# Performance work log

Measured on AMD Instinct MI355X. Metric: run time of the kernel, lower is better.

Reference implementation:

```python
import jax, jax.numpy as jnp
import numpy as np

IMG_H = IMG_W = 800
SIZES = (32, 64, 128, 256, 512)
FEAT_SHAPES = ((200, 200), (100, 100), (50, 50), (25, 25), (13, 13))
ASPECTS = np.array([0.5, 1.0, 2.0], np.float32)
MIN_SIZE = 10.0 / 1000.0
PRE_NMS = 4000
POST_NMS = 1000
IOU_TH = 0.7


def conv2d(x, w, b, pad):
    y = jax.lax.conv_general_dilated(
        x, w, window_strides=(1, 1), padding=[(pad, pad), (pad, pad)],
        dimension_numbers=("NCHW", "OIHW", "NCHW"))
    return y + b[None, :, None, None]


def make_anchors():
    # replicates torchvision AnchorGenerator: per-level single size, 3 aspect ratios
    out = []
    for (gh, gw), s in zip(FEAT_SHAPES, SIZES):
        h_r = np.sqrt(ASPECTS)
        w_r = 1.0 / h_r
        ws = s * w_r
        hs = s * h_r
        base = np.round(np.stack([-ws, -hs, ws, hs], 1) / 2.0)  # [3,4]
        stride_h = IMG_H // gh
        stride_w = IMG_W // gw
        sy = np.arange(gh, dtype=np.float32) * stride_h
        sx = np.arange(gw, dtype=np.float32) * stride_w
        yy, xx = np.meshgrid(sy, sx, indexing="ij")
        shifts = np.stack([xx, yy, xx, yy], axis=-1).reshape(-1, 1, 4)
        out.append((shifts + base[None]).reshape(-1, 4))
    a = np.concatenate(out, 0).astype(np.float32)
    a /= np.array([IMG_W, IMG_H, IMG_W, IMG_H], np.float32)  # normalize to [0,1]
    return jnp.asarray(a)


def xy_to_cxcy(a):
    return jnp.concatenate([(a[:, 2:] + a[:, :2]) / 2, a[:, 2:] - a[:, :2]], 1)


def cxcy_to_xy(a):
    return jnp.concatenate([a[:, :2] - a[:, 2:] / 2, a[:, :2] + a[:, 2:] / 2], 1)


def decode(t, anc):
    return jnp.concatenate([t[:, :2] * anc[:, 2:] + anc[:, :2],
                            jnp.exp(t[:, 2:]) * anc[:, 2:]], 1)


def rpn_head(feat, w_i, b_i, w_c, b_c, w_r, b_r):
    B = feat.shape[0]
    h = jax.nn.relu(conv2d(feat, w_i, b_i, 1))
    c = conv2d(h, w_c, b_c, 0).transpose(0, 2, 3, 1).reshape(B, -1, 2)
    r = conv2d(h, w_r, b_r, 0).transpose(0, 2, 3, 1).reshape(B, -1, 4)
    return c, r


def pairwise_iou(b):
    # b: [N,4] xyxy
    area = jnp.clip(b[:, 2] - b[:, 0], 0) * jnp.clip(b[:, 3] - b[:, 1], 0)
    lt = jnp.maximum(b[:, None, :2], b[None, :, :2])
    rb = jnp.minimum(b[:, None, 2:], b[None, :, 2:])
    wh = jnp.clip(rb - lt, 0)
    inter = wh[..., 0] * wh[..., 1]
    union = area[:, None] + area[None, :] - inter
    return jnp.where(union > 0, inter / union, 0.0)


def greedy_nms(ious, init_keep):
    N = ious.shape[0]
    idxs = jnp.arange(N)

    def body(i, keep):
        sup = keep[i] & (ious[i] > IOU_TH) & (idxs > i)
        return keep & ~sup

    return jax.lax.fori_loop(0, N, body, init_keep)


def rpn_forward(x, feats, w_inter, b_inter, w_cls, b_cls, w_reg, b_reg):
    cls_l, reg_l = [], []
    for f in feats:
        c, r = rpn_head(f, w_inter, b_inter, w_cls, b_cls, w_reg, b_reg)
        cls_l.append(c)
        reg_l.append(r)
    pred_cls = jnp.concatenate(cls_l, 1).reshape(-1, 2)   # [A,2]
    pred_reg = jnp.concatenate(reg_l, 1).reshape(-1, 4)   # [A,4]

    anchor = make_anchors()                               # [A,4] xyxy in [0,1]
    scores = jax.nn.softmax(pred_cls, axis=-1)[:, 1]
    roi = cxcy_to_xy(decode(pred_reg, xy_to_cxcy(anchor))).clip(0.0, 1.0)

    ws = roi[:, 2] - roi[:, 0]
    hs = roi[:, 3] - roi[:, 1]
    valid = (hs >= MIN_SIZE) & (ws >= MIN_SIZE)
    scores = jnp.where(valid, scores, -jnp.inf)

    top_scores, top_idx = jax.lax.top_k(scores, PRE_NMS)
    boxes = roi[top_idx]
    finite = jnp.isfinite(top_scores)
    boxes = jnp.where(finite[:, None], boxes, 0.0)  # neutralize filtered boxes

    ious = pairwise_iou(boxes)
    keep = greedy_nms(ious, finite)
    order = jnp.argsort(jnp.where(keep, jnp.arange(PRE_NMS), PRE_NMS + jnp.arange(PRE_NMS)))
    n_keep = jnp.minimum(keep.sum(), POST_NMS)
    sel = boxes[order[:POST_NMS]]
    roi_out = jnp.where(jnp.arange(POST_NMS)[:, None] < n_keep, sel, 0.0)  # padded [1000,4]
    return pred_cls, pred_reg, roi_out, anchor


def setup_inputs() -> dict:
    key = jax.random.key(0)
    ks = jax.random.split(key, 10)
    inp = {"x": jax.random.normal(ks[0], (1, 3, IMG_H, IMG_W), jnp.float32)}
    for i, (gh, gw) in enumerate(FEAT_SHAPES):
        inp[f"feat{i}"] = jax.random.normal(ks[1 + i], (1, 256, gh, gw), jnp.float32)
    # normal_init(m, 0, 0.01)
    inp["w_inter"] = jax.random.normal(ks[6], (256, 256, 3, 3), jnp.float32) * 0.01
    inp["b_inter"] = jnp.zeros((256,), jnp.float32)
    inp["w_cls"] = jax.random.normal(ks[7], (6, 256, 1, 1), jnp.float32) * 0.01
    inp["b_cls"] = jnp.zeros((6,), jnp.float32)
    inp["w_reg"] = jax.random.normal(ks[8], (12, 256, 1, 1), jnp.float32) * 0.01
    inp["b_reg"] = jnp.zeros((12,), jnp.float32)
    return inp


def reference(x, feat0, feat1, feat2, feat3, feat4,
              w_inter, b_inter, w_cls, b_cls, w_reg, b_reg):
    feats = [feat0, feat1, feat2, feat3, feat4]
    return rpn_forward(x, feats, w_inter, b_inter, w_cls, b_cls, w_reg, b_reg)
```

## Files before the change

kernel.cpp:

```cpp
#include <hip/hip_runtime.h>
#include <cmath>
#include <cstdint>

typedef unsigned int u32;
typedef unsigned long long u64;
typedef float v2f __attribute__((ext_vector_type(2)));

#define A_TOT   159882
#define PRE_NMS 4000
#define POST_NMS 1000
#define NWORDS  63
#define HIST_BINS 131072
#define HIST2_BINS 32768
#define SURV_CAP 8192
#define MONO_NEG_INF 0x007FFFFFu

struct BaseTab { float v[60]; };

__device__ inline u32 mono32f(float s) {
    u32 u = __float_as_uint(s);
    return (u & 0x80000000u) ? ~u : (u | 0x80000000u);
}

__device__ inline float pexp_f(float x0) {
    float x = fminf(x0, 88.3762626647950f);
    x = fmaxf(x, -88.3762626647949f);
    float m = floorf(__builtin_fmaf(x, 1.44269504088896341f, 0.5f));
    float r = __builtin_fmaf(m, -0.693359375f, x);
    r = __builtin_fmaf(m, 2.12194440e-4f, r);
    float z = r * r;
    float y = 1.9875691500E-4f;
    y = __builtin_fmaf(y, r, 1.3981999507E-3f);
    y = __builtin_fmaf(y, r, 8.3334519073E-3f);
    y = __builtin_fmaf(y, r, 4.1665795894E-2f);
    y = __builtin_fmaf(y, r, 1.6666665459E-1f);
    y = __builtin_fmaf(y, r, 5.0000001201E-1f);
    y = __builtin_fmaf(y, z, r);
    y = y + 1.0f;
    return ldexpf(y, (int)m);
}

__device__ inline float4 decode_box(const float* __restrict__ reg,
                                    const float* __restrict__ anc,
                                    u32 i, bool* valid) {
#pragma clang fp contract(off)
    float x1 = anc[4 * i], y1 = anc[4 * i + 1], x2 = anc[4 * i + 2], y2 = anc[4 * i + 3];
    float acx = (x2 + x1) / 2.0f, acy = (y2 + y1) / 2.0f;
    float aw = x2 - x1, ah = y2 - y1;
    float t0 = reg[4 * i], t1 = reg[4 * i + 1], t2 = reg[4 * i + 2], t3 = reg[4 * i + 3];
    float cx = (t0 * aw) + acx;
    float cy = (t1 * ah) + acy;
    float w  = pexp_f(t2) * aw;
    float hh = pexp_f(t3) * ah;
    float bx1 = fminf(fmaxf(cx - w / 2.0f, 0.f), 1.f);
    float by1 = fminf(fmaxf(cy - hh / 2.0f, 0.f), 1.f);
    float bx2 = fminf(fmaxf(cx + w / 2.0f, 0.f), 1.f);
    float by2 = fminf(fmaxf(cy + hh / 2.0f, 0.f), 1.f);
    float wsz = bx2 - bx1, hsz = by2 - by1;
    *valid = (hsz >= 0.01f) && (wsz >= 0.01f);
    return make_float4(bx1, by1, bx2, by2);
}

__device__ inline v2f pk_mul_blo(v2f a, v2f b) {
    v2f d;
    asm("v_pk_mul_f32 %0, %1, %2 op_sel:[0,0] op_sel_hi:[1,0]"
        : "=v"(d) : "v"(a), "v"(b));
    return d;
}
__device__ inline v2f pk_mul_bhi(v2f a, v2f b) {
    v2f d;
    asm("v_pk_mul_f32 %0, %1, %2 op_sel:[0,1] op_sel_hi:[1,1]"
        : "=v"(d) : "v"(a), "v"(b));
    return d;
}
__device__ inline v2f pk_add(v2f a, v2f b) {
    v2f d;
    asm("v_pk_add_f32 %0, %1, %2" : "=v"(d) : "v"(a), "v"(b));
    return d;
}

__device__ inline void gload16(const float* g, void* lds) {
    __builtin_amdgcn_global_load_lds(
        (const __attribute__((address_space(1))) void*)g,
        (__attribute__((address_space(3))) void*)lds,
        16, 0, 0);
}

__global__ __launch_bounds__(256) void wt_k(const float* __restrict__ w,
                                            float* __restrict__ Wt) {
    int i = blockIdx.x * 256 + threadIdx.x;
    if (i >= 2304 * 256) return;
    int co = i & 255, knew = i >> 8;
    int g = knew >> 8;
    int c = knew & 255;
    Wt[knew * 256 + co] = w[co * 2304 + c * 9 + g];
}

struct ConvMap {
    const float* feat[5];
    float* part[5];
    const float* Wt;
    const float* bias;
    u64 M[5];
    int bstart[6];
    int st[5], gh[5], gw[5], S[5], npan[5], fuse[5];
};

__global__ __launch_bounds__(256, 4) void conv_all(ConvMap cm)
{
#pragma clang fp contract(off)
    __shared__ float Ws[2][32][128];
    __shared__ float Xs[2][32][32];
    const int t  = threadIdx.x;
    const int cg = t & 31, xg = t >> 5;
    const int bid = blockIdx.x;
    const int l = (bid >= cm.bstart[1]) + (bid >= cm.bstart[2]) +
                  (bid >= cm.bstart[3]) + (bid >= cm.bstart[4]);
    const int local = bid - cm.bstart[l];
    const int st = cm.st[l], gh = cm.gh[l], gw = cm.gw[l];
    const int S = cm.S[l], npan = cm.npan[l];
    const float* __restrict__ feat = cm.feat[l];
    const float* __restrict__ Wt   = cm.Wt;
    float* __restrict__ part = cm.part[l];
    const int tile = local % st;
    const int zc   = local / st;
    const int s0   = tile * 32;
    const int z2 = zc & 1, pslot = zc >> 1;
    const int pb   = pslot * npan;
    const int send = (pb + npan) * 9;

    const u32 y00 = (u32)(((u64)(u32)s0 * cm.M[l]) >> 48);
    const int x00 = s0 - (int)y00 * gw;
    int xq = x00 + cg;
    int yq = (int)y00;
#pragma unroll
    for (int r = 0; r < 3; ++r) { if (xq >= gw) { xq -= gw; ++yq; } }

    const int srow0 = t >> 5;
    const int wcol  = (t & 31) << 2;
    const int wvoff = (t >> 6) * 1024;

    float px0, px1, px2, px3;

#define ISSUE_X(s_) do {                                                       \
        int g_  = (s_) >> 3, cb_ = ((s_) & 7) << 5;                            \
        int ky_ = g_ / 3, kx_ = g_ - ky_ * 3;                                  \
        int yy_ = yq + ky_ - 1;                                                \
        int xx_ = xq + kx_ - 1;                                                \
        bool ok_ = (yy_ >= 0) && (yy_ < gh) && (xx_ >= 0) && (xx_ < gw);       \
        int yyc_ = ok_ ? yy_ : 0;                                              \
        int xcc_ = ok_ ? xx_ : 0;                                              \
        const float* xsrc_ = feat + ((size_t)(cb_ + srow0) * gh + yyc_) * gw   \
                                  + xcc_;                                      \
        size_t xstr_ = (size_t)(8 * gh) * gw;                                  \
        float xa_ = xsrc_[0];                                                  \
        float xb_ = xsrc_[xstr_];                                              \
        float xc2_ = xsrc_[2 * xstr_];                                         \
        float xd_ = xsrc_[3 * xstr_];                                          \
        px0 = ok_ ? xa_ : 0.f;                                                 \
        px1 = ok_ ? xb_ : 0.f;                                                 \
        px2 = ok_ ? xc2_ : 0.f;                                                \
        px3 = ok_ ? xd_ : 0.f;                                                 \
    } while (0)

#define COMMIT_X(b_) do {                                                      \
        Xs[b_][srow0][cg]      = px0;                                          \
        Xs[b_][srow0 + 8][cg]  = px1;                                          \
        Xs[b_][srow0 + 16][cg] = px2;                                          \
        Xs[b_][srow0 + 24][cg] = px3;                                          \
    } while (0)

#define ISSUE_W(s_, b_) do {                                                   \
        int g_  = (s_) >> 3, cb_ = ((s_) & 7) << 5;                            \
        const float* wsrc_ = Wt + ((size_t)(g_ * 256 + cb_ + srow0) * 256)     \
                               + z2 * 128 + wcol;                              \
        char* ldsW_ = (char*)(&Ws[b_][0][0]) + wvoff;                          \
        gload16(wsrc_,        ldsW_);                                          \
        gload16(wsrc_ + 2048, ldsW_ + 4096);                                   \
        gload16(wsrc_ + 4096, ldsW_ + 8192);                                   \
        gload16(wsrc_ + 6144, ldsW_ + 12288);                                  \
    } while (0)

    v2f tA0=(v2f)0.f, tA1=(v2f)0.f, tA2=(v2f)0.f, tA3=(v2f)0.f;
    v2f tB0=(v2f)0.f, tB1=(v2f)0.f, tB2=(v2f)0.f, tB3=(v2f)0.f;

    const int sfirst = pb * 9;
    ISSUE_X(sfirst);
    COMMIT_X(0);
    ISSUE_W(sfirst, 0);
    ISSUE_X(sfirst + 1);
    __syncthreads();
    int cur = 0;

    for (int pi = pb; pi < pb + npan; ++pi) {
        v2f pA0=(v2f)0.f, pA1=(v2f)0.f, pA2=(v2f)0.f, pA3=(v2f)0.f;
        v2f pB0=(v2f)0.f, pB1=(v2f)0.f, pB2=(v2f)0.f, pB3=(v2f)0.f;
        for (int j = 0; j < 9; ++j) {
            int s = pi * 9 + j;
            int nxt = cur ^ 1;
            bool more = (s + 1 < send);
            if (more) {
                COMMIT_X(nxt);
                ISSUE_W(s + 1, nxt);
                if (s + 2 < send) ISSUE_X(s + 2);
            }
            const float* Wb = &Ws[cur][0][0];
            const float* Xb = &Xs[cur][0][0];
#pragma unroll 4
            for (int kk = 0; kk < 32; ++kk) {
                float4 xv = *(const float4*)(Xb + kk * 32 + xg * 4);
                v2f xlo; xlo[0] = xv.x; xlo[1] = xv.y;
                v2f xhi; xhi[0] = xv.z; xhi[1] = xv.w;
                v2f wA = *(const v2f*)(Wb + kk * 128 + cg * 2);
                pA0 = pk_add(pA0, pk_mul_blo(wA, xlo));
                pA1 = pk_add(pA1, pk_mul_bhi(wA, xlo));
                pA2 = pk_add(pA2, pk_mul_blo(wA, xhi));
                pA3 = pk_add(pA3, pk_mul_bhi(wA, xhi));
                v2f wB = *(const v2f*)(Wb + kk * 128 + 64 + cg * 2);
                pB0 = pk_add(pB0, pk_mul_blo(wB, xlo));
                pB1 = pk_add(pB1, pk_mul_bhi(wB, xlo));
                pB2 = pk_add(pB2, pk_mul_blo(wB, xhi));
                pB3 = pk_add(pB3, pk_mul_bhi(wB, xhi));
            }
            if (more) {
                __syncthreads();
                cur = nxt;
            }
        }
        tA0 = pk_add(tA0, pA0); tA1 = pk_add(tA1, pA1);
        tA2 = pk_add(tA2, pA2); tA3 = pk_add(tA3, pA3);
        tB0 = pk_add(tB0, pB0); tB1 = pk_add(tB1, pB1);
        tB2 = pk_add(tB2, pB2); tB3 = pk_add(tB3, pB3);
    }
#undef ISSUE_X
#undef COMMIT_X
#undef ISSUE_W
    const int c0 = z2 * 128 + cg * 2;
    if (cm.fuse[l]) {
        const float* bias = cm.bias;
        float bA0 = bias[c0], bA1 = bias[c0 + 1];
        float bB0 = bias[c0 + 64], bB1 = bias[c0 + 65];
        tA0[0] = fmaxf(tA0[0] + bA0, 0.f); tA0[1] = fmaxf(tA0[1] + bA1, 0.f);
        tA1[0] = fmaxf(tA1[0] + bA0, 0.f); tA1[1] = fmaxf(tA1[1] + bA1, 0.f);
        tA2[0] = fmaxf(tA2[0] + bA0, 0.f); tA2[1] = fmaxf(tA2[1] + bA1, 0.f);
        tA3[0] = fmaxf(tA3[0] + bA0, 0.f); tA3[1] = fmaxf(tA3[1] + bA1, 0.f);
        tB0[0] = fmaxf(tB0[0] + bB0, 0.f); tB0[1] = fmaxf(tB0[1] + bB1, 0.f);
        tB1[0] = fmaxf(tB1[0] + bB0, 0.f); tB1[1] = fmaxf(tB1[1] + bB1, 0.f);
        tB2[0] = fmaxf(tB2[0] + bB0, 0.f); tB2[1] = fmaxf(tB2[1] + bB1, 0.f);
        tB3[0] = fmaxf(tB3[0] + bB0, 0.f); tB3[1] = fmaxf(tB3[1] + bB1, 0.f);
    }
    float* op = part + (size_t)pslot * 256 * S;
    {
        int sp = s0 + xg * 4;
        size_t rA0 = (size_t)c0 * S + sp;
        size_t rA1 = rA0 + S;
        if (sp + 0 < S) { op[rA0 + 0] = tA0[0]; op[rA1 + 0] = tA0[1]; }
        if (sp + 1 < S) { op[rA0 + 1] = tA1[0]; op[rA1 + 1] = tA1[1]; }
        if (sp + 2 < S) { op[rA0 + 2] = tA2[0]; op[rA1 + 2] = tA2[1]; }
        if (sp + 3 < S) { op[rA0 + 3] = tA3[0]; op[rA1 + 3] = tA3[1]; }
        size_t rB0 = rA0 + (size_t)64 * S;
        size_t rB1 = rB0 + S;
        if (sp + 0 < S) { op[rB0 + 0] = tB0[0]; op[rB1 + 0] = tB0[1]; }
        if (sp + 1 < S) { op[rB0 + 1] = tB1[0]; op[rB1 + 1] = tB1[1]; }
        if (sp + 2 < S) { op[rB0 + 2] = tB2[0]; op[rB1 + 2] = tB2[1]; }
        if (sp + 3 < S) { op[rB0 + 3] = tB3[0]; op[rB1 + 3] = tB3[1]; }
    }
}

struct HeadMap {
    const float* h[5];
    int S[5], abase[5], npan[5], bstart[6];
};

__global__ __launch_bounds__(256) void head_all(
    HeadMap hm, const float* __restrict__ wc,
    const float* __restrict__ bc, const float* __restrict__ wr,
    const float* __restrict__ br, const float* __restrict__ bias,
    float* __restrict__ cls_out, float* __restrict__ reg_out)
{
#pragma clang fp contract(off)
    int bid = blockIdx.x;
    int l = (bid >= hm.bstart[1]) + (bid >= hm.bstart[2]) +
            (bid >= hm.bstart[3]) + (bid >= hm.bstart[4]);
    int local = bid - hm.bstart[l];
    const float* __restrict__ h = hm.h[l];
    const int S = hm.S[l];
    const int abase = hm.abase[l];
    const int npan = hm.npan[l];
    int s = local * 256 + threadIdx.x;
    if (s >= S) return;
    float ac[6]  = {0.f};
    float ar[12] = {0.f};
    for (int c = 0; c < 256; ++c) {
        size_t i = (size_t)c * S + s;
        float v;
        if (npan == 1) {
            v = h[i];
        } else {
            float vv = h[i];
            for (int p = 1; p < 8; ++p)
                vv = vv + h[(size_t)p * 256 * S + i];
            v = fmaxf(vv + bias[c], 0.f);
        }
#pragma unroll
        for (int ch = 0; ch < 6; ++ch) {
            float prod = wc[ch * 256 + c] * v;
            ac[ch] = ac[ch] + prod;
        }
#pragma unroll
        for (int ch = 0; ch < 12; ++ch) {
            float prod = wr[ch * 256 + c] * v;
            ar[ch] = ar[ch] + prod;
        }
    }
    long b2 = (long)abase + (long)s * 3;
#pragma unroll
    for (int a = 0; a < 3; ++a) {
#pragma unroll
        for (int c2 = 0; c2 < 2; ++c2)
            cls_out[(b2 + a) * 2 + c2] = ac[a * 2 + c2] + bc[a * 2 + c2];
#pragma unroll
        for (int d = 0; d < 4; ++d)
            reg_out[(b2 + a) * 4 + d] = ar[a * 4 + d] + br[a * 4 + d];
    }
}

__global__ __launch_bounds__(256) void score_k(
    const float* __restrict__ cls, const float* __restrict__ reg,
    BaseTab bt, u64* __restrict__ keys, u32* __restrict__ hist,
    float* __restrict__ anc_out)
{
#pragma clang fp contract(off)
    int i = blockIdx.x * 256 + threadIdx.x;
    if (i >= A_TOT) return;
    int l, base, gw, str;
    if (i < 120000)      { l = 0; base = 0;      gw = 200; str = 4;  }
    else if (i < 150000) { l = 1; base = 120000; gw = 100; str = 8;  }
    else if (i < 157500) { l = 2; base = 150000; gw = 50;  str = 16; }
    else if (i < 159375) { l = 3; base = 157500; gw = 25;  str = 32; }
    else                 { l = 4; base = 159375; gw = 13;  str = 61; }
    int j = i - base;
    int sj = j / 3;
    int a = j - sj * 3;
    int yy = sj / gw;
    int xx = sj - yy * gw;
    float sx = (float)(xx * str), sy = (float)(yy * str);
    const float* bb = &bt.v[(l * 3 + a) * 4];
    float a0 = (sx + bb[0]) / 800.0f;
    float a1 = (sy + bb[1]) / 800.0f;
    float a2 = (sx + bb[2]) / 800.0f;
    float a3 = (sy + bb[3]) / 800.0f;
    anc_out[4 * i + 0] = a0;
    anc_out[4 * i + 1] = a1;
    anc_out[4 * i + 2] = a2;
    anc_out[4 * i + 3] = a3;
    float l0 = cls[2 * i], l1 = cls[2 * i + 1];
    float m  = fmaxf(l0, l1);
    float e0 = pexp_f(l0 - m);
    float e1 = pexp_f(l1 - m);
    float sum = e0 + e1;
    float sc  = e1 / sum;
    float acx = (a2 + a0) / 2.0f, acy = (a3 + a1) / 2.0f;
    float aw = a2 - a0, ah = a3 - a1;
    float t0 = reg[4 * i], t1 = reg[4 * i + 1], t2 = reg[4 * i + 2], t3 = reg[4 * i + 3];
    float cx = (t0 * aw) + acx;
    float cy = (t1 * ah) + acy;
    float w  = pexp_f(t2) * aw;
    float hh = pexp_f(t3) * ah;
    float bx1 = fminf(fmaxf(cx - w / 2.0f, 0.f), 1.f);
    float by1 = fminf(fmaxf(cy - hh / 2.0f, 0.f), 1.f);
    float bx2 = fminf(fmaxf(cx + w / 2.0f, 0.f), 1.f);
    float by2 = fminf(fmaxf(cy + hh / 2.0f, 0.f), 1.f);
    float wsz = bx2 - bx1, hsz = by2 - by1;
    bool valid = (hsz >= 0.01f) && (wsz >= 0.01f);

    float score = valid ? sc : -INFINITY;
    u32 u = mono32f(score);
    keys[i] = ((u64)u << 32) | (u32)(~(u32)i);
    atomicAdd(&hist[u >> 15], 1u);
}

__global__ __launch_bounds__(1024) void topk_thresh(const u32* __restrict__ hist,
                                                    u32* __restrict__ counters) {
    __shared__ u32 part[1024];
    int t = threadIdx.x;
    u32 s = 0;
    for (int q = 0; q < 128; ++q) s += hist[HIST_BINS - 1 - (t * 128 + q)];
    part[t] = s;
    __syncthreads();
    if (t == 0) {
        u32 cum = 0, cumBefore = 0;
        int tc = 1023;
        for (int c = 0; c < 1024; ++c) {
            if (cum + part[c] >= PRE_NMS) { tc = c; cumBefore = cum; break; }
            cum += part[c];
        }
        u32 cum2 = cumBefore;
        int bstar = 0;
        for (int q = 0; q < 128; ++q) {
            int b = HIST_BINS - 1 - (tc * 128 + q);
            u32 hv = hist[b];
            if (cum2 + hv >= PRE_NMS) { bstar = b; break; }
            cum2 += hv;
        }
        counters[0] = (u32)bstar;
        counters[1] = cum2;
    }
}

__global__ __launch_bounds__(256) void hist2_k(const u64* __restrict__ keys,
                                               const u32* __restrict__ counters,
                                               u32* __restrict__ hist2) {
    int i = blockIdx.x * 256 + threadIdx.x;
    if (i >= A_TOT) return;
    u32 u = (u32)(keys[i] >> 32);
    if ((u >> 15) == counters[0]) atomicAdd(&hist2[u & 0x7FFF], 1u);
}

__global__ __launch_bounds__(1024) void thresh2_k(const u32* __restrict__ hist2,
                                                  u32* __restrict__ counters) {
    __shared__ u32 part[1024];
    int t = threadIdx.x;
    u32 s = 0;
    for (int q = 0; q < 32; ++q) s += hist2[HIST2_BINS - 1 - (t * 32 + q)];
    part[t] = s;
    __syncthreads();
    if (t == 0) {
        u32 bstar = counters[0];
        u32 cum = counters[1];
        int tc = 1023;
        u32 cumBefore = cum;
        for (int c = 0; c < 1024; ++c) {
            if (cum + part[c] >= PRE_NMS) { tc = c; cumBefore = cum; break; }
            cum += part[c];
        }
        u32 cum2 = cumBefore;
        u32 low = 0;
        for (int q = 0; q < 32; ++q) {
            int b = HIST2_BINS - 1 - (tc * 32 + q);
            u32 hv = hist2[b];
            if (cum2 + hv >= PRE_NMS) { low = (u32)b; break; }
            cum2 += hv;
        }
        counters[3] = (bstar << 15) | low;
    }
}

__global__ __launch_bounds__(256) void compact_k(const u64* __restrict__ keys,
                                                 u32* __restrict__ counters,
                                                 u64* __restrict__ surv) {
    int i = blockIdx.x * 256 + threadIdx.x;
    if (i >= A_TOT) return;
    u32 cut = counters[3];
    u64 k = keys[i];
    if ((u32)(k >> 32) >= cut) {
        u32 slot = atomicAdd(&counters[2], 1u);
        if (slot < SURV_CAP) surv[slot] = k;
    }
}

__global__ __launch_bounds__(1024) void sort_topk(
    const u64* __restrict__ surv, const u32* __restrict__ counters,
    const float* __restrict__ reg, const float* __restrict__ anc,
    float* __restrict__ boxes4k, u64* __restrict__ finmask)
{
    __shared__ u64 K[SURV_CAP];
    int t = threadIdx.x;
    u32 n = counters[2];
    if (n > SURV_CAP) n = SURV_CAP;
    for (int p = t; p < SURV_CAP; p += 1024) K[p] = (p < (int)n) ? surv[p] : 0ull;
    __syncthreads();
    for (int k = 2; k <= SURV_CAP; k <<= 1) {
        for (int j = k >> 1; j > 0; j >>= 1) {
            for (int p = t; p < SURV_CAP / 2; p += 1024) {
                int i = 2 * p - (p & (j - 1));
                int pr = i + j;
                bool desc = ((i & k) == 0);
                u64 a = K[i], b = K[pr];
                if (desc ? (a < b) : (a > b)) { K[i] = b; K[pr] = a; }
            }
            __syncthreads();
        }
    }
    for (int jj = t; jj < PRE_NMS; jj += 1024) {
        u64 key = K[jj];
        u32 u = (u32)(key >> 32);
        float b0 = 0.f, b1 = 0.f, b2 = 0.f, b3 = 0.f;
        if (u > MONO_NEG_INF) {
            u32 idx = ~(u32)key;
            bool valid;
            float4 bx = decode_box(reg, anc, idx, &valid);
            b0 = bx.x; b1 = bx.y; b2 = bx.z; b3 = bx.w;
        }
        boxes4k[4 * jj + 0] = b0;
        boxes4k[4 * jj + 1] = b1;
        boxes4k[4 * jj + 2] = b2;
        boxes4k[4 * jj + 3] = b3;
    }
    if (t < NWORDS) {
        u64 wmask = 0;
        for (int b = 0; b < 64; ++b) {
            int jj = t * 64 + b;
            if (jj < PRE_NMS) {
                u32 u = (u32)(K[jj] >> 32);
                if (u > MONO_NEG_INF) wmask |= (1ull << b);
            }
        }
        finmask[t] = wmask;
    }
}

__global__ __launch_bounds__(64) void supmat_k(const float* __restrict__ boxes4k,
                                               u64* __restrict__ sup) {
#pragma clang fp contract(off)
    __shared__ float cb[64][4];
    int rb = blockIdx.y, cbk = blockIdx.x;
    int tl = threadIdx.x;
    int j = cbk * 64 + tl;
    if (j < PRE_NMS) {
        cb[tl][0] = boxes4k[4 * j + 0];
        cb[tl][1] = boxes4k[4 * j + 1];
        cb[tl][2] = boxes4k[4 * j + 2];
        cb[tl][3] = boxes4k[4 * j + 3];
    } else {
        cb[tl][0] = cb[tl][1] = cb[tl][2] = cb[tl][3] = 0.f;
    }
    __syncthreads();
    int i = rb * 64 + tl;
    if (i >= PRE_NMS) return;
    float ax1 = boxes4k[4 * i + 0], ay1 = boxes4k[4 * i + 1];
    float ax2 = boxes4k[4 * i + 2], ay2 = boxes4k[4 * i + 3];
    float aarea = fmaxf(ax2 - ax1, 0.f) * fmaxf(ay2 - ay1, 0.f);
    u64 w = 0;
    for (int q = 0; q < 64; ++q) {
        int jg = cbk * 64 + q;
        if (jg >= PRE_NMS || jg <= i) continue;
        float bx1 = cb[q][0], by1 = cb[q][1], bx2 = cb[q][2], by2 = cb[q][3];
        float barea = fmaxf(bx2 - bx1, 0.f) * fmaxf(by2 - by1, 0.f);
        float lx = fmaxf(ax1, bx1), ly = fmaxf(ay1, by1);
        float rx = fminf(ax2, bx2), ry = fminf(ay2, by2);
        float iw = fmaxf(rx - lx, 0.f), ih = fmaxf(ry - ly, 0.f);
        float inter = iw * ih;
        float uni = (aarea + barea) - inter;
        float iou = (uni > 0.f) ? inter / uni : 0.f;
        if (iou > 0.7f) w |= (1ull << q);
    }
    sup[(size_t)i * NWORDS + cbk] = w;
}

__device__ inline u64 shfl_u64(u64 v, int lane) {
    int lo = __shfl((int)(u32)(v & 0xFFFFFFFFull), lane, 64);
    int hi = __shfl((int)(u32)(v >> 32), lane, 64);
    return ((u64)(u32)hi << 32) | (u32)lo;
}

__global__ __launch_bounds__(64) void nms_scan_k(const u64* __restrict__ sup,
                                                 const u64* __restrict__ finmask,
                                                 u64* __restrict__ keepw) {
    int lane = threadIdx.x;
    u64 keep = (lane < NWORDS) ? finmask[lane] : 0ull;
    u64 cur[8], nxt[8];
#pragma unroll
    for (int q = 0; q < 8; ++q)
        cur[q] = (lane < NWORDS) ? sup[(size_t)q * NWORDS + lane] : 0ull;
    for (int base = 0; base < PRE_NMS; base += 8) {
        int nb = base + 8;
#pragma unroll
        for (int q = 0; q < 8; ++q) {
            int i = nb + q;
            nxt[q] = (lane < NWORDS && i < PRE_NMS) ? sup[(size_t)i * NWORDS + lane] : 0ull;
        }
#pragma unroll
        for (int q = 0; q < 8; ++q) {
            int i = base + q;
            int wi = i >> 6, bi = i & 63;
            u64 kw = shfl_u64(keep, wi);
            if ((kw >> bi) & 1ull) keep &= ~cur[q];
        }
#pragma unroll
        for (int q = 0; q < 8; ++q) cur[q] = nxt[q];
    }
    if (lane < NWORDS) keepw[lane] = keep;
}

__global__ __launch_bounds__(1024) void output_k(const u64* __restrict__ keepw,
                                                 const float* __restrict__ boxes4k,
                                                 float* __restrict__ roi_out) {
    __shared__ u32 pref[NWORDS + 1];
    int t = threadIdx.x;
    if (t == 0) {
        u32 run = 0;
        for (int w = 0; w < NWORDS; ++w) { pref[w] = run; run += (u32)__popcll(keepw[w]); }
        pref[NWORDS] = run;
    }
    __syncthreads();
    u32 total = pref[NWORDS];
    u32 nk = total < (u32)POST_NMS ? total : (u32)POST_NMS;
    for (int j = t; j < PRE_NMS; j += 1024) {
        int wi = j >> 6, bi = j & 63;
        u64 kw = keepw[wi];
        if ((kw >> bi) & 1ull) {
            u32 rank = pref[wi] + (u32)__popcll(kw & ((1ull << bi) - 1ull));
            if (rank < (u32)POST_NMS) {
                roi_out[4 * rank + 0] = boxes4k[4 * j + 0];
                roi_out[4 * rank + 1] = boxes4k[4 * j + 1];
                roi_out[4 * rank + 2] = boxes4k[4 * j + 2];
                roi_out[4 * rank + 3] = boxes4k[4 * j + 3];
            }
        }
    }
    for (int r2 = t; r2 < POST_NMS; r2 += 1024) {
        if ((u32)r2 >= nk) {
            roi_out[4 * r2 + 0] = 0.f;
            roi_out[4 * r2 + 1] = 0.f;
            roi_out[4 * r2 + 2] = 0.f;
            roi_out[4 * r2 + 3] = 0.f;
        }
    }
}

extern "C" void kernel_launch(void* const* d_in, const int* in_sizes, int n_in,
                              void* d_out, int out_size, void* d_ws, size_t ws_size,
                              hipStream_t stream) {
    const float* feat[5] = {
        (const float*)d_in[1], (const float*)d_in[2], (const float*)d_in[3],
        (const float*)d_in[4], (const float*)d_in[5]};
    const float* w_inter = (const float*)d_in[6];
    const float* b_inter = (const float*)d_in[7];
    const float* w_cls   = (const float*)d_in[8];
    const float* b_cls   = (const float*)d_in[9];
    const float* w_reg   = (const float*)d_in[10];
    const float* b_reg   = (const float*)d_in[11];

    float* out     = (float*)d_out;
    float* out_cls = out;
    float* out_reg = out + 319764;
    float* out_roi = out + 959292;
    float* out_anc = out + 963292;

    static const int GH[5]    = {200, 100, 50, 25, 13};
    static const int GW[5]    = {200, 100, 50, 25, 13};
    static const int SL[5]    = {40000, 10000, 2500, 625, 169};
    static const int ABASE[5] = {0, 120000, 150000, 157500, 159375};
    static const int NPAN_ST[5] = {1, 1, 8, 8, 8};

    char* p = (char*)d_ws;
    size_t off = 0;
    auto alloc = [&](size_t bytes) -> void* {
        void* r = p + off;
        off = (off + bytes + 255) & ~(size_t)255;
        return r;
    };
    float* Wt      = (float*)alloc((size_t)2304 * 256 * 4);
    float* part[5];
    for (int l = 0; l < 5; ++l)
        part[l] = (float*)alloc((size_t)NPAN_ST[l] * 256 * SL[l] * 4);
    u64*   keys    = (u64*)  alloc((size_t)A_TOT * 8);
    u32*   hist    = (u32*)  alloc((size_t)HIST_BINS * 4);
    u32*   hist2   = (u32*)  alloc((size_t)HIST2_BINS * 4);
    u32*   counters= (u32*)  alloc(256);
    u64*   surv    = (u64*)  alloc((size_t)SURV_CAP * 8);
    float* boxes4k = (float*)alloc((size_t)PRE_NMS * 4 * 4);
    u64*   finmask = (u64*)  alloc(64 * 8);
    u64*   supmat  = (u64*)  alloc((size_t)PRE_NMS * NWORDS * 8);
    u64*   keepw   = (u64*)  alloc(64 * 8);
    (void)ws_size;

    BaseTab bt;
    {
        const float sizes[5] = {32.f, 64.f, 128.f, 256.f, 512.f};
        const float asp[3] = {0.5f, 1.0f, 2.0f};
        for (int l = 0; l < 5; ++l)
            for (int a = 0; a < 3; ++a) {
                float hr = sqrtf(asp[a]);
                float wr = 1.0f / hr;
                float wsf = sizes[l] * wr;
                float hsf = sizes[l] * hr;
                bt.v[(l * 3 + a) * 4 + 0] = rintf(-wsf / 2.0f);
                bt.v[(l * 3 + a) * 4 + 1] = rintf(-hsf / 2.0f);
                bt.v[(l * 3 + a) * 4 + 2] = rintf( wsf / 2.0f);
                bt.v[(l * 3 + a) * 4 + 3] = rintf( hsf / 2.0f);
            }
    }

    hipMemsetAsync(hist, 0, (size_t)HIST_BINS * 4, stream);
    hipMemsetAsync(hist2, 0, (size_t)HIST2_BINS * 4, stream);
    hipMemsetAsync(counters, 0, 256, stream);

    wt_k<<<2304, 256, 0, stream>>>(w_inter, Wt);

    ConvMap cm;
    cm.Wt = Wt;
    cm.bias = b_inter;
    int bacc = 0;
    for (int l = 0; l < 5; ++l) {
        cm.feat[l] = feat[l];
        cm.part[l] = part[l];
        int st = (SL[l] + 31) / 32;
        cm.st[l] = st; cm.gh[l] = GH[l]; cm.gw[l] = GW[l]; cm.S[l] = SL[l];
        cm.M[l] = (((u64)1 << 48) + (u64)GW[l] - 1) / (u64)GW[l];
        int zsplit = NPAN_ST[l];
        cm.npan[l] = (zsplit == 1) ? 8 : 1;
        cm.fuse[l] = (zsplit == 1) ? 1 : 0;
        cm.bstart[l] = bacc;
        bacc += st * (zsplit * 2);
    }
    cm.bstart[5] = bacc;
    conv_all<<<bacc, 256, 0, stream>>>(cm);

    HeadMap hm;
    int hacc = 0;
    for (int l = 0; l < 5; ++l) {
        hm.h[l] = part[l];
        hm.S[l] = SL[l];
        hm.abase[l] = ABASE[l];
        hm.npan[l] = NPAN_ST[l];
        hm.bstart[l] = hacc;
        hacc += (SL[l] + 255) / 256;
    }
    hm.bstart[5] = hacc;
    head_all<<<hacc, 256, 0, stream>>>(hm, w_cls, b_cls, w_reg, b_reg,
                                       b_inter, out_cls, out_reg);

    int nbA = (A_TOT + 255) / 256;
    score_k<<<nbA, 256, 0, stream>>>(out_cls, out_reg, bt, keys, hist, out_anc);
    topk_thresh<<<1, 1024, 0, stream>>>(hist, counters);
    hist2_k<<<nbA, 256, 0, stream>>>(keys, counters, hist2);
    thresh2_k<<<1, 1024, 0, stream>>>(hist2, counters);
    compact_k<<<nbA, 256, 0, stream>>>(keys, counters, surv);
    sort_topk<<<1, 1024, 0, stream>>>(surv, counters, out_reg, out_anc, boxes4k, finmask);
    supmat_k<<<dim3(NWORDS, NWORDS), 64, 0, stream>>>(boxes4k, supmat);
    nms_scan_k<<<1, 64, 0, stream>>>(supmat, finmask, keepw);
    output_k<<<1, 1024, 0, stream>>>(keepw, boxes4k, out_roi);
}
```

Measured before the change: 2.472 ms.

## Fold memsets into weight transpose, merge NMS scan with output, shrink sort

Replaces the three hipMemsetAsync calls by zeroing the histograms and counters inside the weight-transpose kernel. The NMS scan and output compaction become one kernel that keeps the keep-mask in shared memory, and the scan prefetches three row groups ahead instead of one. The bitonic sort in sort_topk uses a 4096-element network when the survivor count fits, halving its passes. These cut launch and memset overhead and serial latency on the single-block tail, at the cost of extra registers for the deeper prefetch.

```diff
diff --git a/kernel.cpp b/kernel.cpp
--- a/kernel.cpp
+++ b/kernel.cpp
@@ -87,8 +87,14 @@
 }
 
 __global__ __launch_bounds__(256) void wt_k(const float* __restrict__ w,
-                                            float* __restrict__ Wt) {
+                                            float* __restrict__ Wt,
+                                            u32* __restrict__ hist,
+                                            u32* __restrict__ hist2,
+                                            u32* __restrict__ counters) {
     int i = blockIdx.x * 256 + threadIdx.x;
+    if (i < HIST_BINS) hist[i] = 0;
+    if (i < HIST2_BINS) hist2[i] = 0;
+    if (i < 64) counters[i] = 0;
     if (i >= 2304 * 256) return;
     int co = i & 255, knew = i >> 8;
     int g = knew >> 8;
@@ -468,11 +474,12 @@
     int t = threadIdx.x;
     u32 n = counters[2];
     if (n > SURV_CAP) n = SURV_CAP;
-    for (int p = t; p < SURV_CAP; p += 1024) K[p] = (p < (int)n) ? surv[p] : 0ull;
+    const int msize = (n <= 4096) ? 4096 : SURV_CAP;
+    for (int p = t; p < msize; p += 1024) K[p] = (p < (int)n) ? surv[p] : 0ull;
     __syncthreads();
-    for (int k = 2; k <= SURV_CAP; k <<= 1) {
+    for (int k = 2; k <= msize; k <<= 1) {
         for (int j = k >> 1; j > 0; j >>= 1) {
-            for (int p = t; p < SURV_CAP / 2; p += 1024) {
+            for (int p = t; p < msize / 2; p += 1024) {
                 int i = 2 * p - (p & (j - 1));
                 int pr = i + j;
                 bool desc = ((i & k) == 0);
@@ -554,51 +561,54 @@
     return ((u64)(u32)hi << 32) | (u32)lo;
 }
 
-__global__ __launch_bounds__(64) void nms_scan_k(const u64* __restrict__ sup,
+__global__ __launch_bounds__(256) void nms_out_k(const u64* __restrict__ sup,
                                                  const u64* __restrict__ finmask,
-                                                 u64* __restrict__ keepw) {
-    int lane = threadIdx.x;
-    u64 keep = (lane < NWORDS) ? finmask[lane] : 0ull;
-    u64 cur[8], nxt[8];
-#pragma unroll
-    for (int q = 0; q < 8; ++q)
-        cur[q] = (lane < NWORDS) ? sup[(size_t)q * NWORDS + lane] : 0ull;
-    for (int base = 0; base < PRE_NMS; base += 8) {
-        int nb = base + 8;
-#pragma unroll
-        for (int q = 0; q < 8; ++q) {
-            int i = nb + q;
-            nxt[q] = (lane < NWORDS && i < PRE_NMS) ? sup[(size_t)i * NWORDS + lane] : 0ull;
-        }
-#pragma unroll
-        for (int q = 0; q < 8; ++q) {
-            int i = base + q;
-            int wi = i >> 6, bi = i & 63;
-            u64 kw = shfl_u64(keep, wi);
-            if ((kw >> bi) & 1ull) keep &= ~cur[q];
-        }
-#pragma unroll
-        for (int q = 0; q < 8; ++q) cur[q] = nxt[q];
-    }
-    if (lane < NWORDS) keepw[lane] = keep;
-}
-
-__global__ __launch_bounds__(1024) void output_k(const u64* __restrict__ keepw,
                                                  const float* __restrict__ boxes4k,
                                                  float* __restrict__ roi_out) {
+    __shared__ u64 keepw_s[NWORDS];
     __shared__ u32 pref[NWORDS + 1];
     int t = threadIdx.x;
+    if (t < 64) {
+        int lane = t;
+        u64 keep = (lane < NWORDS) ? finmask[lane] : 0ull;
+        u64 cur[8], n1[8], n2[8], nw[8];
+#define LDROW(dst_, i0_)                                                       \
+        _Pragma("unroll")                                                      \
+        for (int q = 0; q < 8; ++q) {                                          \
+            int i_ = (i0_) + q;                                                \
+            dst_[q] = (lane < NWORDS && i_ < PRE_NMS)                          \
+                      ? sup[(size_t)i_ * NWORDS + lane] : 0ull;                \
+        }
+        LDROW(cur, 0)
+        LDROW(n1, 8)
+        LDROW(n2, 16)
+        for (int base = 0; base < PRE_NMS; base += 8) {
+            LDROW(nw, base + 24)
+#pragma unroll
+            for (int q = 0; q < 8; ++q) {
+                int i = base + q;
+                int wi = i >> 6, bi = i & 63;
+                u64 kw = shfl_u64(keep, wi);
+                if ((kw >> bi) & 1ull) keep &= ~cur[q];
+            }
+#pragma unroll
+            for (int q = 0; q < 8; ++q) { cur[q] = n1[q]; n1[q] = n2[q]; n2[q] = nw[q]; }
+        }
+#undef LDROW
+        if (lane < NWORDS) keepw_s[lane] = keep;
+    }
+    __syncthreads();
     if (t == 0) {
         u32 run = 0;
-        for (int w = 0; w < NWORDS; ++w) { pref[w] = run; run += (u32)__popcll(keepw[w]); }
+        for (int w = 0; w < NWORDS; ++w) { pref[w] = run; run += (u32)__popcll(keepw_s[w]); }
         pref[NWORDS] = run;
     }
     __syncthreads();
     u32 total = pref[NWORDS];
     u32 nk = total < (u32)POST_NMS ? total : (u32)POST_NMS;
-    for (int j = t; j < PRE_NMS; j += 1024) {
+    for (int j = t; j < PRE_NMS; j += 256) {
         int wi = j >> 6, bi = j & 63;
-        u64 kw = keepw[wi];
+        u64 kw = keepw_s[wi];
         if ((kw >> bi) & 1ull) {
             u32 rank = pref[wi] + (u32)__popcll(kw & ((1ull << bi) - 1ull));
             if (rank < (u32)POST_NMS) {
@@ -609,7 +619,7 @@
             }
         }
     }
-    for (int r2 = t; r2 < POST_NMS; r2 += 1024) {
+    for (int r2 = t; r2 < POST_NMS; r2 += 256) {
         if ((u32)r2 >= nk) {
             roi_out[4 * r2 + 0] = 0.f;
             roi_out[4 * r2 + 1] = 0.f;
@@ -663,7 +673,6 @@
     float* boxes4k = (float*)alloc((size_t)PRE_NMS * 4 * 4);
     u64*   finmask = (u64*)  alloc(64 * 8);
     u64*   supmat  = (u64*)  alloc((size_t)PRE_NMS * NWORDS * 8);
-    u64*   keepw   = (u64*)  alloc(64 * 8);
     (void)ws_size;
 
     BaseTab bt;
@@ -683,11 +692,7 @@
             }
     }
 
-    hipMemsetAsync(hist, 0, (size_t)HIST_BINS * 4, stream);
-    hipMemsetAsync(hist2, 0, (size_t)HIST2_BINS * 4, stream);
-    hipMemsetAsync(counters, 0, 256, stream);
-
-    wt_k<<<2304, 256, 0, stream>>>(w_inter, Wt);
+    wt_k<<<2304, 256, 0, stream>>>(w_inter, Wt, hist, hist2, counters);
 
     ConvMap cm;
     cm.Wt = Wt;
@@ -730,6 +735,5 @@
     compact_k<<<nbA, 256, 0, stream>>>(keys, counters, surv);
     sort_topk<<<1, 1024, 0, stream>>>(surv, counters, out_reg, out_anc, boxes4k, finmask);
     supmat_k<<<dim3(NWORDS, NWORDS), 64, 0, stream>>>(boxes4k, supmat);
-    nms_scan_k<<<1, 64, 0, stream>>>(supmat, finmask, keepw);
-    output_k<<<1, 1024, 0, stream>>>(keepw, boxes4k, out_roi);
-}
+    nms_out_k<<<1, 256, 0, stream>>>(supmat, finmask, boxes4k, out_roi);
+}
```

Result: faster. 2.403 ms, median of 2 (-2.8%).
